# Kernel optimization log

Measured on AMD Instinct MI355X. Metric: run time of the kernel, lower is better.

## Reference

```python
import jax, jax.numpy as jnp
import numpy as np

B, C, H, W = 8, 96, 256, 256
PATCH, DIM, HEAD = 2, 384, 4
D = DIM // HEAD          # 96, minGRU feature dim
K = 2 * PATCH + 1        # 5, patch-embed kernel
GK = 3                   # positional conv kernel


def setup_inputs() -> dict:
    key = jax.random.key(0)
    ks = jax.random.split(key, 16)
    w = lambda k, shape: jax.random.normal(k, shape, jnp.float32) * 0.02
    return {
        'x': jax.random.normal(ks[0], (B, C, H, W), jnp.float32),
        'r_pw': w(ks[1], (DIM, C, K, K)),            # Conv2d weight (out,in,kh,kw)
        'r_pb': w(ks[2], (DIM,)),
        'c_pw': w(ks[3], (DIM, C, K, K)),
        'c_pb': w(ks[4], (DIM,)),
        'r_pe_w': w(ks[5], (DIM, DIM // C, GK, GK)),  # grouped conv, groups=C
        'r_pe_b': w(ks[6], (DIM,)),
        'c_pe_w': w(ks[7], (DIM, DIM // C, GK, GK)),
        'c_pe_b': w(ks[8], (DIM,)),
        'r_un_w': w(ks[9], (DIM, C, PATCH, PATCH)),   # ConvTranspose2d weight (in,out,kh,kw)
        'r_un_b': w(ks[10], (C,)),
        'c_un_w': w(ks[11], (DIM, C, PATCH, PATCH)),
        'c_un_b': w(ks[12], (C,)),
        'r_gru_w': w(ks[13], (D, 2 * D)),             # minGRU to_hidden_and_gate (no bias)
        'c_gru_w': w(ks[14], (D, 2 * D)),
    }


def _conv(x, w, b, stride, pad, groups=1):
    y = jax.lax.conv_general_dilated(
        x, w, (stride, stride), [(pad, pad), (pad, pad)],
        dimension_numbers=('NCHW', 'OIHW', 'NCHW'), feature_group_count=groups)
    return y + b[None, :, None, None]


def _min_gru(seq, w):
    # seq: (N, S, D); log-space parallel scan (heinsen scan), lucidrains minGRU
    hg = seq @ w                                  # (N, S, 2D)
    hidden, gate = jnp.split(hg, 2, axis=-1)
    log_coeffs = -jax.nn.softplus(gate)           # log(1 - z)
    log_z = -jax.nn.softplus(-gate)               # log z
    log_tilde_h = jnp.where(hidden >= 0,
                            jnp.log(jax.nn.relu(hidden) + 0.5),
                            -jax.nn.softplus(-hidden))
    a_star = jnp.cumsum(log_coeffs, axis=1)
    log_h = a_star + jax.lax.cumlogsumexp(log_z + log_tilde_h - a_star, axis=1)
    return jnp.exp(log_h)


def _unpatch(x, w, b):
    # ConvTranspose2d with kernel==stride==PATCH, pad=0: pure block expansion
    Bq, Ci, Hp, Wp = x.shape
    y = jnp.einsum('bchw,copq->bohpwq', x, w).reshape(Bq, w.shape[1], Hp * PATCH, Wp * PATCH)
    return y + b[None, :, None, None]


def reference(x, r_pw, r_pb, c_pw, c_pb, r_pe_w, r_pe_b, c_pe_w, c_pe_b,
              r_un_w, r_un_b, c_un_w, c_un_b, r_gru_w, c_gru_w):
    r = _conv(x, r_pw, r_pb, PATCH, PATCH)        # (B, DIM, Hp, Wp)
    c = _conv(x, c_pw, c_pb, PATCH, PATCH)
    r_pe = _conv(r, r_pe_w, r_pe_b, 1, 1, groups=C)
    c_pe = _conv(c, c_pe_w, c_pe_b, 1, 1, groups=C)
    Bq, _, Hp, Wp = r.shape
    # row scan: (B,head,D,Hp,Wp) -> (B,head,Wp,Hp,D) -> scan over Hp
    r = r.reshape(Bq, HEAD, D, Hp, Wp).transpose(0, 1, 4, 3, 2).reshape(-1, Hp, D)
    # col scan: (B,head,D,Hp,Wp) -> (B,head,Hp,Wp,D) -> scan over Wp
    c = c.reshape(Bq, HEAD, D, Hp, Wp).transpose(0, 1, 3, 4, 2).reshape(-1, Wp, D)
    r = _min_gru(r, r_gru_w)
    c = _min_gru(c, c_gru_w)
    r = r.reshape(Bq, HEAD, Wp, Hp, D).transpose(0, 1, 4, 3, 2).reshape(Bq, DIM, Hp, Wp)
    c = c.reshape(Bq, HEAD, Hp, Wp, D).transpose(0, 1, 4, 2, 3).reshape(Bq, DIM, Hp, Wp)
    return _unpatch(r + r_pe, r_un_w, r_un_b) + _unpatch(c + c_pe, c_un_w, c_un_b)
```

## Files before the change

kernel.cpp:

```cpp
#include <hip/hip_runtime.h>
#include <stdint.h>
#include <stdio.h>

typedef __attribute__((ext_vector_type(8))) short short8;
typedef __attribute__((ext_vector_type(4))) float f32x4;
typedef __attribute__((ext_vector_type(4))) unsigned int u32x4;
typedef __attribute__((ext_vector_type(4))) unsigned short u16x4;

#define DEV static __device__ __forceinline__

DEV unsigned short f2bf(float f){
  unsigned u = __float_as_uint(f);
  u += 0x7FFFu + ((u >> 16) & 1u);
  return (unsigned short)(u >> 16);
}
DEV float bf2f(unsigned short h){ return __uint_as_float(((unsigned)h) << 16); }

__global__ __launch_bounds__(256) void k_xt(const float* __restrict__ x,
                                            unsigned short* __restrict__ xt){
  int bid = blockIdx.x;
  int wq = bid & 3, h = (bid >> 2) & 255, b = bid >> 10;
  int w0 = wq * 64;
  __shared__ unsigned short s[64 * 104];
  int t = threadIdx.x;
  int wl = t & 63, cq = t >> 6;
  const float* xp = x + ((size_t)b * 96 * 256 + h) * 256 + w0 + wl;
  #pragma unroll
  for (int i = 0; i < 24; ++i){
    int c = cq + i * 4;
    s[wl * 104 + c] = f2bf(xp[(size_t)c * 65536]);
  }
  __syncthreads();
  unsigned short* dst = xt + (((size_t)b * 260 + h + 2) * 260 + (w0 + 2)) * 128;
  #pragma unroll
  for (int p = 0; p < 3; ++p){
    int i = t + p * 256;
    int w = i / 12, ch = i % 12;
    u32x4 v = *(const u32x4*)&s[w * 104 + ch * 8];
    *(u32x4*)&dst[(size_t)w * 128 + ch * 8] = v;
  }
}

__global__ __launch_bounds__(256) void k_pack(const float* __restrict__ rpw, const float* __restrict__ cpw,
    const float* __restrict__ runw, const float* __restrict__ cunw,
    const float* __restrict__ runb, const float* __restrict__ cunb,
    const float* __restrict__ rgw,  const float* __restrict__ cgw,
    unsigned short* __restrict__ A2, unsigned short* __restrict__ Aun,
    unsigned short* __restrict__ Agr, float* __restrict__ bun){
  int tid = blockIdx.x * 256 + threadIdx.x;
  const int NA2 = 768 * 2400, NUN = 384 * 768, NGR = 2 * 192 * 96;
  if (tid < NA2){
    int oc = tid / 2400, r = tid % 2400;
    int kh = r / 480, kw = (r / 96) % 5, ic = r % 96;
    const float* W = oc < 384 ? rpw : cpw;
    int o = oc < 384 ? oc : oc - 384;
    A2[tid] = f2bf(W[(((size_t)o * 96 + ic) * 5 + kh) * 5 + kw]);
  } else if (tid < NA2 + NUN){
    int i = tid - NA2;
    int m = i / 768, ci = i % 768;
    int co = m >> 2, p = (m >> 1) & 1, q = m & 1;
    const float* W = ci < 384 ? runw : cunw;
    int c = ci < 384 ? ci : ci - 384;
    Aun[i] = f2bf(W[(((size_t)c * 96 + co) * 2 + p) * 2 + q]);
  } else if (tid < NA2 + NUN + NGR){
    int i = tid - NA2 - NUN;
    int side = i / 18432, r = i % 18432;
    int m = r / 96, k = r % 96;
    const float* W = side ? cgw : rgw;
    Agr[i] = f2bf(W[k * 192 + m]);
  } else if (tid < NA2 + NUN + NGR + 96){
    int co = tid - NA2 - NUN - NGR;
    bun[co] = runb[co] + cunb[co];
  }
}

__global__ __launch_bounds__(512) void k_conv(const unsigned short* __restrict__ xt,
    const unsigned short* __restrict__ A2,
    const float* __restrict__ rpb, const float* __restrict__ cpb,
    unsigned short* __restrict__ cl){
  __shared__ char lds[160768];
  const int BOFF = 26624;
  const int BPITCH = 33536;
  const int BITEMS = 8384;
  int t = threadIdx.x, lane = t & 63;
  int wid = t >> 6, mw = wid >> 2, nw = wid & 3;
  int wl = lane & 15, cg = lane >> 4;
  int bid = blockIdx.x;
  int xcd = bid & 7, rr = bid >> 3;
  int mt = rr % 6, pgrp = rr / 6;
  int p = pgrp * 8 + xcd;
  int wq = p & 1, hq = (p >> 1) & 31, b = p >> 6;
  int ho0 = hq * 4, wo0 = wq * 64;
  int M0 = mt * 128;

  int a_oc = t >> 2, a_q = t & 3;
  const unsigned short* Aoc = A2 + (size_t)(M0 + a_oc) * 2400 + a_q * 24;
  char* Adst = lds + a_oc * 208 + a_q * 48;

  f32x4 acc[4][4];
  #pragma unroll
  for (int i = 0; i < 4; ++i)
    #pragma unroll
    for (int j = 0; j < 4; ++j) acc[i][j] = (f32x4){0.f, 0.f, 0.f, 0.f};

  u32x4 aR[3], bR[17];
  #pragma unroll
  for (int c = 0; c < 3; ++c) aR[c] = *(const u32x4*)(Aoc + c * 8);
  #pragma unroll
  for (int it = 0; it < 17; ++it){
    int i = t + it * 512;
    if (i < BITEMS){
      int row = i / 2096, j = i % 2096, col = j >> 4, ch = j & 15;
      bR[it] = *(const u32x4*)&xt[(((size_t)b * 260 + 2 * ho0 + 2 * row) * 260 + 2 * wo0 + col) * 128 + ch * 8];
    }
  }
  #pragma unroll
  for (int c = 0; c < 3; ++c) *(u32x4*)(Adst + c * 16) = aR[c];
  #pragma unroll
  for (int it = 0; it < 17; ++it){
    int i = t + it * 512;
    if (i < BITEMS){
      int row = i / 2096, j = i % 2096, col = j >> 4, ch = j & 15;
      *(u32x4*)(lds + BOFF + row * BPITCH + col * 256 + (ch ^ ((col >> 1) & 7)) * 16) = bR[it];
    }
  }
  __syncthreads();

  for (int kh = 0; kh < 5; ++kh){
    #pragma unroll
    for (int kw = 0; kw < 5; ++kw){
      bool last = (kh == 4 && kw == 4);
      bool khb  = (kw == 4 && kh < 4);
      if (!last){
        int nkh = kh + (kw == 4 ? 1 : 0), nkw = (kw == 4 ? 0 : kw + 1);
        const unsigned short* As = Aoc + (nkh * 5 + nkw) * 96;
        #pragma unroll
        for (int c = 0; c < 3; ++c) aR[c] = *(const u32x4*)(As + c * 8);
      }
      if (khb){
        #pragma unroll
        for (int it = 0; it < 17; ++it){
          int i = t + it * 512;
          if (i < BITEMS){
            int row = i / 2096, j = i % 2096, col = j >> 4, ch = j & 15;
            bR[it] = *(const u32x4*)&xt[(((size_t)b * 260 + 2 * ho0 + 2 * row + kh + 1) * 260 + 2 * wo0 + col) * 128 + ch * 8];
          }
        }
      }
      {
        int col = 32 * nw + 2 * wl + kw;
        int sx = (col >> 1) & 7;
        #pragma unroll
        for (int ics = 0; ics < 3; ++ics){
          short8 af[4], bfr[4];
          #pragma unroll
          for (int mf = 0; mf < 4; ++mf)
            af[mf] = *(const short8*)(lds + (mw * 64 + mf * 16 + wl) * 208 + ics * 64 + cg * 16);
          int chl = (ics * 4 + cg) ^ sx;
          #pragma unroll
          for (int nf = 0; nf < 4; ++nf)
            bfr[nf] = *(const short8*)(lds + BOFF + nf * BPITCH + col * 256 + chl * 16);
          #pragma unroll
          for (int mf = 0; mf < 4; ++mf)
            #pragma unroll
            for (int nf = 0; nf < 4; ++nf)
              acc[mf][nf] = __builtin_amdgcn_mfma_f32_16x16x32_bf16(af[mf], bfr[nf], acc[mf][nf], 0, 0, 0);
        }
      }
      __syncthreads();
      if (!last){
        #pragma unroll
        for (int c = 0; c < 3; ++c) *(u32x4*)(Adst + c * 16) = aR[c];
        if (khb){
          #pragma unroll
          for (int it = 0; it < 17; ++it){
            int i = t + it * 512;
            if (i < BITEMS){
              int row = i / 2096, j = i % 2096, col = j >> 4, ch = j & 15;
              *(u32x4*)(lds + BOFF + row * BPITCH + col * 256 + (ch ^ ((col >> 1) & 7)) * 16) = bR[it];
            }
          }
        }
      }
      __syncthreads();
    }
  }
  unsigned short* S = (unsigned short*)lds;
  #pragma unroll
  for (int mf = 0; mf < 4; ++mf)
    #pragma unroll
    for (int nf = 0; nf < 4; ++nf){
      int wol = nw * 16 + wl;
      int pxl = nf * 64 + wol;
      int sw8 = (pxl & 7) << 3;
      #pragma unroll
      for (int j = 0; j < 4; ++j){
        int ocl = mw * 64 + mf * 16 + cg * 4 + j;
        int oc = M0 + ocl;
        float v = acc[mf][nf][j] + (oc < 384 ? rpb[oc] : cpb[oc - 384]);
        S[pxl * 128 + (ocl ^ sw8)] = f2bf(v);
      }
    }
  __syncthreads();
  #pragma unroll
  for (int it = 0; it < 8; ++it){
    int i = t + it * 512;
    int pxl = i >> 4, ch = i & 15;
    int chs = ch ^ (pxl & 7);
    int ho = ho0 + (pxl >> 6), wo = wo0 + (pxl & 63);
    u32x4 v = *(const u32x4*)&S[pxl * 128 + chs * 8];
    *(u32x4*)&cl[(((size_t)b * 128 + ho) * 128 + wo) * 768 + M0 + ch * 8] = v;
  }
}

__global__ __launch_bounds__(256) void k_pe(const unsigned short* __restrict__ cl,
    const float* __restrict__ rpew, const float* __restrict__ cpew,
    const float* __restrict__ rpeb, const float* __restrict__ cpeb,
    unsigned short* __restrict__ sum){
  __shared__ unsigned short si[340 * 52];
  __shared__ float sw[48 * 36];
  __shared__ float sb[48];
  int bid = blockIdx.x;
  int wq = bid & 3, hq = (bid >> 2) & 15, slab = (bid >> 6) & 15, b = bid >> 10;
  int ch0 = slab * 48, hp0 = hq * 8, wp0 = wq * 32;
  int t = threadIdx.x;
  for (int i = t; i < 48 * 36; i += 256){
    int ocl = i / 36, r = i % 36;
    int oc = ch0 + ocl;
    const float* W = oc < 384 ? rpew : cpew;
    int o = oc < 384 ? oc : oc - 384;
    sw[i] = W[(size_t)o * 36 + r];
  }
  if (t < 48){
    int oc = ch0 + t;
    sb[t] = oc < 384 ? rpeb[oc] : cpeb[oc - 384];
  }
  for (int i = t; i < 340 * 24; i += 256){
    int pix = i / 24, c2 = i % 24;
    int r2 = pix / 34, cc = pix % 34;
    int hp = hp0 - 1 + r2, wp = wp0 - 1 + cc;
    unsigned v = 0;
    if (hp >= 0 && hp < 128 && wp >= 0 && wp < 128)
      v = *(const unsigned*)&cl[((size_t)b * 16384 + hp * 128 + wp) * 768 + ch0 + c2 * 2];
    *(unsigned*)&si[pix * 52 + c2 * 2] = v;
  }
  __syncthreads();
  int hpl = t >> 5, wpl = t & 31;
  unsigned int outp[24];
  #pragma unroll
  for (int g = 0; g < 12; ++g){
    float o0 = sb[g * 4], o1 = sb[g * 4 + 1], o2 = sb[g * 4 + 2], o3 = sb[g * 4 + 3];
    #pragma unroll
    for (int dh = 0; dh < 3; ++dh)
      #pragma unroll
      for (int dw = 0; dw < 3; ++dw){
        int pix = (hpl + dh) * 34 + (wpl + dw);
        u16x4 v = *(const u16x4*)&si[pix * 52 + g * 4];
        float x0 = bf2f(v[0]), x1 = bf2f(v[1]), x2 = bf2f(v[2]), x3 = bf2f(v[3]);
        int r = dh * 3 + dw;
        o0 = fmaf(sw[(g*4+0)*36 + 0*9 + r], x0, o0); o0 = fmaf(sw[(g*4+0)*36 + 1*9 + r], x1, o0);
        o0 = fmaf(sw[(g*4+0)*36 + 2*9 + r], x2, o0); o0 = fmaf(sw[(g*4+0)*36 + 3*9 + r], x3, o0);
        o1 = fmaf(sw[(g*4+1)*36 + 0*9 + r], x0, o1); o1 = fmaf(sw[(g*4+1)*36 + 1*9 + r], x1, o1);
        o1 = fmaf(sw[(g*4+1)*36 + 2*9 + r], x2, o1); o1 = fmaf(sw[(g*4+1)*36 + 3*9 + r], x3, o1);
        o2 = fmaf(sw[(g*4+2)*36 + 0*9 + r], x0, o2); o2 = fmaf(sw[(g*4+2)*36 + 1*9 + r], x1, o2);
        o2 = fmaf(sw[(g*4+2)*36 + 2*9 + r], x2, o2); o2 = fmaf(sw[(g*4+2)*36 + 3*9 + r], x3, o2);
        o3 = fmaf(sw[(g*4+3)*36 + 0*9 + r], x0, o3); o3 = fmaf(sw[(g*4+3)*36 + 1*9 + r], x1, o3);
        o3 = fmaf(sw[(g*4+3)*36 + 2*9 + r], x2, o3); o3 = fmaf(sw[(g*4+3)*36 + 3*9 + r], x3, o3);
      }
    outp[g * 2]     = (unsigned)f2bf(o0) | ((unsigned)f2bf(o1) << 16);
    outp[g * 2 + 1] = (unsigned)f2bf(o2) | ((unsigned)f2bf(o3) << 16);
  }
  size_t obase = (((size_t)b * 128 + hp0 + hpl) * 128 + wp0 + wpl) * 768 + ch0;
  #pragma unroll
  for (int c6 = 0; c6 < 6; ++c6){
    u32x4 v = { outp[c6 * 4], outp[c6 * 4 + 1], outp[c6 * 4 + 2], outp[c6 * 4 + 3] };
    *(u32x4*)&sum[obase + c6 * 8] = v;
  }
}

__global__ __launch_bounds__(256) void k_gruf(const unsigned short* __restrict__ cl,
    const unsigned short* __restrict__ Agr, unsigned short* __restrict__ sum){
  __shared__ char lds[78848];
  const int AOFF = 0, BOFF2 = 39936, HOFF = 53248;
  int t = threadIdx.x, lane = t & 63, wid = t >> 6;
  int wl = lane & 15, cg = lane >> 4;
  int bid = blockIdx.x;
  int cb = bid & 7, head = (bid >> 3) & 3, b = (bid >> 5) & 7, side = bid >> 8;
  size_t clbase = ((size_t)b * 16384) * 768 + side * 384 + head * 96;
  for (int i = t; i < 2304; i += 256){
    int m = i / 12, c = i % 12;
    u32x4 v = *(const u32x4*)&Agr[((size_t)side * 192 + m) * 96 + c * 8];
    *(u32x4*)(lds + AOFF + m * 208 + c * 16) = v;
  }
  for (int i = t; i < 768; i += 256){
    int px = i / 12, c = i % 12;
    int s = px >> 4, xl = px & 15;
    int xg = cb * 16 + xl;
    int pxg = side ? (xg * 128 + s) : (s * 128 + xg);
    u32x4 v = *(const u32x4*)&cl[clbase + (size_t)pxg * 768 + c * 8];
    *(u32x4*)(lds + BOFF2 + px * 208 + c * 16) = v;
  }
  int s_chain = t & 15, s_dg = t >> 4;
  float h[8];
  #pragma unroll
  for (int k = 0; k < 8; ++k) h[k] = 0.f;
  __syncthreads();

  for (int ch = 0; ch < 32; ++ch){
    int s0 = ch * 4;
    f32x4 acc[12];
    #pragma unroll
    for (int i = 0; i < 12; ++i) acc[i] = (f32x4){0.f, 0.f, 0.f, 0.f};
    #pragma unroll
    for (int ks = 0; ks < 3; ++ks){
      short8 bf = *(const short8*)(lds + BOFF2 + (wid * 16 + wl) * 208 + ks * 64 + cg * 16);
      #pragma unroll
      for (int mf = 0; mf < 12; ++mf){
        short8 af = *(const short8*)(lds + AOFF + (mf * 16 + wl) * 208 + ks * 64 + cg * 16);
        acc[mf] = __builtin_amdgcn_mfma_f32_16x16x32_bf16(af, bf, acc[mf], 0, 0, 0);
      }
    }
    {
      int px = wid * 16 + wl;
      #pragma unroll
      for (int mf = 0; mf < 12; ++mf){
        unsigned p0 = (unsigned)f2bf(acc[mf][0]) | ((unsigned)f2bf(acc[mf][1]) << 16);
        unsigned p1 = (unsigned)f2bf(acc[mf][2]) | ((unsigned)f2bf(acc[mf][3]) << 16);
        unsigned long long pp = (unsigned long long)p0 | ((unsigned long long)p1 << 32);
        *(unsigned long long*)(lds + HOFF + px * 400 + (mf * 16 + cg * 4) * 2) = pp;
      }
    }
    __syncthreads();
    if (s_dg < 12){
      #pragma unroll
      for (int s = 0; s < 4; ++s){
        int px = s * 16 + s_chain;
        short8 hid8 = *(const short8*)(lds + HOFF + px * 400 + s_dg * 16);
        short8 gat8 = *(const short8*)(lds + HOFF + px * 400 + 192 + s_dg * 16);
        int xg = cb * 16 + s_chain;
        int pxg = side ? (xg * 128 + (s0 + s)) : ((s0 + s) * 128 + xg);
        unsigned short* sp = (unsigned short*)&sum[clbase + (size_t)pxg * 768 + s_dg * 8];
        u32x4 sv = *(u32x4*)sp;
        unsigned short* svp = (unsigned short*)&sv;
        #pragma unroll
        for (int k = 0; k < 8; ++k){
          float hid = bf2f((unsigned short)hid8[k]);
          float gat = bf2f((unsigned short)gat8[k]);
          float z  = 1.f / (1.f + __expf(-gat));
          float th = hid >= 0.f ? hid + 0.5f : 1.f / (1.f + __expf(-hid));
          h[k] += z * (th - h[k]);
          svp[k] = f2bf(bf2f(svp[k]) + h[k]);
        }
        *(u32x4*)sp = sv;
      }
    }
    if (ch < 31){
      int sn = (ch + 1) * 4;
      for (int i = t; i < 768; i += 256){
        int px = i / 12, c = i % 12;
        int s = px >> 4, xl = px & 15;
        int xg = cb * 16 + xl;
        int pxg = side ? (xg * 128 + (sn + s)) : ((sn + s) * 128 + xg);
        u32x4 v = *(const u32x4*)&cl[clbase + (size_t)pxg * 768 + c * 8];
        *(u32x4*)(lds + BOFF2 + px * 208 + c * 16) = v;
      }
    }
    __syncthreads();
  }
}

__global__ __launch_bounds__(256) void k_unpatch(const unsigned short* __restrict__ sum,
    const unsigned short* __restrict__ Aun, const float* __restrict__ bun,
    float* __restrict__ out){
  __shared__ char lds[53248];
  int t = threadIdx.x, lane = t & 63;
  int wid = t >> 6, mw = wid >> 1, nw = wid & 1;
  int bid = blockIdx.x;
  int xcd = bid & 7, rr = bid >> 3;
  int mt = rr % 3, pgrp = rr / 3;
  int M0 = mt * 128;
  size_t N0 = (size_t)(pgrp * 8 + xcd) * 128;
  f32x4 acc[4][4];
  #pragma unroll
  for (int i = 0; i < 4; ++i)
    #pragma unroll
    for (int j = 0; j < 4; ++j) acc[i][j] = (f32x4){0.f, 0.f, 0.f, 0.f};
  for (int kc = 0; kc < 8; ++kc){
    __syncthreads();
    for (int i = t; i < 1536; i += 256){
      int m = i / 12, c = i % 12;
      u32x4 v = *(const u32x4*)&Aun[(size_t)(M0 + m) * 768 + kc * 96 + c * 8];
      *(u32x4*)(lds + m * 208 + c * 16) = v;
    }
    for (int i = t; i < 1536; i += 256){
      int px = i / 12, c = i % 12;
      u32x4 v = *(const u32x4*)&sum[(N0 + px) * 768 + kc * 96 + c * 8];
      *(u32x4*)(lds + 26624 + px * 208 + c * 16) = v;
    }
    __syncthreads();
    #pragma unroll
    for (int ks = 0; ks < 3; ++ks){
      short8 af[4], bfr[4];
      #pragma unroll
      for (int mf = 0; mf < 4; ++mf)
        af[mf] = *(const short8*)(lds + (mw * 64 + mf * 16 + (lane & 15)) * 208 + ks * 64 + (lane >> 4) * 16);
      #pragma unroll
      for (int nf = 0; nf < 4; ++nf)
        bfr[nf] = *(const short8*)(lds + 26624 + (nw * 64 + nf * 16 + (lane & 15)) * 208 + ks * 64 + (lane >> 4) * 16);
      #pragma unroll
      for (int mf = 0; mf < 4; ++mf)
        #pragma unroll
        for (int nf = 0; nf < 4; ++nf)
          acc[mf][nf] = __builtin_amdgcn_mfma_f32_16x16x32_bf16(af[mf], bfr[nf], acc[mf][nf], 0, 0, 0);
    }
  }
  #pragma unroll
  for (int mf = 0; mf < 4; ++mf)
    #pragma unroll
    for (int nf = 0; nf < 4; ++nf)
      #pragma unroll
      for (int j = 0; j < 4; ++j){
        int m = M0 + mw * 64 + mf * 16 + (lane >> 4) * 4 + j;
        int co = m >> 2, p = (m >> 1) & 1, q = m & 1;
        size_t px = N0 + nw * 64 + nf * 16 + (lane & 15);
        int b = (int)(px >> 14); int pxl = (int)(px & 16383);
        int hp = pxl >> 7, wp = pxl & 127;
        out[(((size_t)b * 96 + co) * 256 + 2 * hp + p) * 256 + 2 * wp + q] = acc[mf][nf][j] + bun[co];
      }
}

extern "C" void kernel_launch(void* const* d_in, const int* in_sizes, int n_in,
                              void* d_out, int out_size, void* d_ws, size_t ws_size,
                              hipStream_t stream){
  (void)in_sizes; (void)n_in; (void)out_size;
  const float* x    = (const float*)d_in[0];
  const float* rpw  = (const float*)d_in[1];
  const float* rpb  = (const float*)d_in[2];
  const float* cpw  = (const float*)d_in[3];
  const float* cpb  = (const float*)d_in[4];
  const float* rpew = (const float*)d_in[5];
  const float* rpeb = (const float*)d_in[6];
  const float* cpew = (const float*)d_in[7];
  const float* cpeb = (const float*)d_in[8];
  const float* runw = (const float*)d_in[9];
  const float* runb = (const float*)d_in[10];
  const float* cunw = (const float*)d_in[11];
  const float* cunb = (const float*)d_in[12];
  const float* rgw  = (const float*)d_in[13];
  const float* cgw  = (const float*)d_in[14];

  char* ws = (char*)d_ws;
  const size_t SZ_XT   = (size_t)8 * 260 * 260 * 128 * 2;
  const size_t OFF_A2  = SZ_XT;
  const size_t SZ_A2   = (size_t)768 * 2400 * 2;
  const size_t OFF_AUN = OFF_A2 + SZ_A2;
  const size_t SZ_AUN  = (size_t)384 * 768 * 2;
  const size_t OFF_AGR = OFF_AUN + SZ_AUN;
  const size_t SZ_AGR  = (size_t)2 * 192 * 96 * 2;
  const size_t OFF_BUN = OFF_AGR + SZ_AGR;
  const size_t OFF_HG  = ((OFF_BUN + 384) + 255) & ~(size_t)255;
  const size_t SZ_PL   = (size_t)8 * 768 * 128 * 128 * 2;
  const size_t OFF_CL  = OFF_HG + SZ_PL;
  const size_t OFF_SUM = OFF_CL + SZ_PL;
  const size_t NEED    = OFF_SUM + SZ_PL;
  if (ws_size < NEED){
    fprintf(stderr, "kernel_launch: ws_size %zu < needed %zu\n", ws_size, NEED);
    return;
  }
  unsigned short* xt  = (unsigned short*)(ws);
  unsigned short* A2  = (unsigned short*)(ws + OFF_A2);
  unsigned short* Aun = (unsigned short*)(ws + OFF_AUN);
  unsigned short* Agr = (unsigned short*)(ws + OFF_AGR);
  float*          bun = (float*)(ws + OFF_BUN);
  unsigned short* cl  = (unsigned short*)(ws + OFF_CL);
  unsigned short* sum = (unsigned short*)(ws + OFF_SUM);
  float* out = (float*)d_out;

  hipMemsetAsync(xt, 0, SZ_XT, stream);
  k_xt  <<<dim3(8192),    dim3(256), 0, stream>>>(x, xt);
  k_pack<<<dim3(8497),    dim3(256), 0, stream>>>(rpw, cpw, runw, cunw, runb, cunb, rgw, cgw, A2, Aun, Agr, bun);
  k_conv<<<dim3(3072),    dim3(512), 0, stream>>>(xt, A2, rpb, cpb, cl);
  k_pe  <<<dim3(8192),    dim3(256), 0, stream>>>(cl, rpew, cpew, rpeb, cpeb, sum);
  k_gruf<<<dim3(512),     dim3(256), 0, stream>>>(cl, Agr, sum);
  k_unpatch<<<dim3(3072), dim3(256), 0, stream>>>(sum, Aun, bun, out);
}
```

Measured before the change: 1.690 ms.

## Load conv weights directly from pre-swizzled global layout and halve conv block tile

After: 2.063 ms. 1.22x slower.

```diff
diff --git a/kernel.cpp b/kernel.cpp
--- a/kernel.cpp
+++ b/kernel.cpp
@@ -4,6 +4,7 @@
 
 typedef __attribute__((ext_vector_type(8))) short short8;
 typedef __attribute__((ext_vector_type(4))) float f32x4;
+typedef __attribute__((ext_vector_type(2))) float f32x2;
 typedef __attribute__((ext_vector_type(4))) unsigned int u32x4;
 typedef __attribute__((ext_vector_type(4))) unsigned short u16x4;
 
@@ -45,57 +46,59 @@
     const float* __restrict__ runw, const float* __restrict__ cunw,
     const float* __restrict__ runb, const float* __restrict__ cunb,
     const float* __restrict__ rgw,  const float* __restrict__ cgw,
-    unsigned short* __restrict__ A2, unsigned short* __restrict__ Aun,
+    unsigned short* __restrict__ A3, unsigned short* __restrict__ Aun,
     unsigned short* __restrict__ Agr, float* __restrict__ bun){
   int tid = blockIdx.x * 256 + threadIdx.x;
-  const int NA2 = 768 * 2400, NUN = 384 * 768, NGR = 2 * 192 * 96;
-  if (tid < NA2){
-    int oc = tid / 2400, r = tid % 2400;
-    int kh = r / 480, kw = (r / 96) % 5, ic = r % 96;
+  const int NA3 = 768 * 2400, NUN = 384 * 768, NGR = 2 * 192 * 96;
+  if (tid < NA3){
+    int e = tid & 7, lane = (tid >> 3) & 63, mf = (tid >> 9) & 3, mw = (tid >> 11) & 1;
+    int r = tid >> 12;
+    int ics = r % 3, r2 = r / 3;
+    int s = r2 % 25, mt = r2 / 25;
+    int kh = s / 5, kw = s % 5;
+    int oc = mt * 128 + mw * 64 + mf * 16 + (lane & 15);
+    int ic = ics * 32 + (lane >> 4) * 8 + e;
     const float* W = oc < 384 ? rpw : cpw;
     int o = oc < 384 ? oc : oc - 384;
-    A2[tid] = f2bf(W[(((size_t)o * 96 + ic) * 5 + kh) * 5 + kw]);
-  } else if (tid < NA2 + NUN){
-    int i = tid - NA2;
+    A3[tid] = f2bf(W[(((size_t)o * 96 + ic) * 5 + kh) * 5 + kw]);
+  } else if (tid < NA3 + NUN){
+    int i = tid - NA3;
     int m = i / 768, ci = i % 768;
     int co = m >> 2, p = (m >> 1) & 1, q = m & 1;
     const float* W = ci < 384 ? runw : cunw;
     int c = ci < 384 ? ci : ci - 384;
     Aun[i] = f2bf(W[(((size_t)c * 96 + co) * 2 + p) * 2 + q]);
-  } else if (tid < NA2 + NUN + NGR){
-    int i = tid - NA2 - NUN;
+  } else if (tid < NA3 + NUN + NGR){
+    int i = tid - NA3 - NUN;
     int side = i / 18432, r = i % 18432;
     int m = r / 96, k = r % 96;
     const float* W = side ? cgw : rgw;
     Agr[i] = f2bf(W[k * 192 + m]);
-  } else if (tid < NA2 + NUN + NGR + 96){
-    int co = tid - NA2 - NUN - NGR;
+  } else if (tid < NA3 + NUN + NGR + 96){
+    int co = tid - NA3 - NUN - NGR;
     bun[co] = runb[co] + cunb[co];
   }
 }
 
-__global__ __launch_bounds__(512) void k_conv(const unsigned short* __restrict__ xt,
-    const unsigned short* __restrict__ A2,
+__global__ __launch_bounds__(256) void k_conv(const unsigned short* __restrict__ xt,
+    const unsigned short* __restrict__ A3,
     const float* __restrict__ rpb, const float* __restrict__ cpb,
     unsigned short* __restrict__ cl){
-  __shared__ char lds[160768];
-  const int BOFF = 26624;
+  __shared__ char lds[67072];
   const int BPITCH = 33536;
-  const int BITEMS = 8384;
+  const int BITEMS = 3144;
   int t = threadIdx.x, lane = t & 63;
-  int wid = t >> 6, mw = wid >> 2, nw = wid & 3;
+  int wid = t >> 6, mw = wid >> 1, nw = wid & 1;
   int wl = lane & 15, cg = lane >> 4;
   int bid = blockIdx.x;
   int xcd = bid & 7, rr = bid >> 3;
   int mt = rr % 6, pgrp = rr / 6;
   int p = pgrp * 8 + xcd;
-  int wq = p & 1, hq = (p >> 1) & 31, b = p >> 6;
-  int ho0 = hq * 4, wo0 = wq * 64;
+  int wq = p & 1, hq = (p >> 1) & 63, b = p >> 7;
+  int ho0 = hq * 2, wo0 = wq * 64;
   int M0 = mt * 128;
 
-  int a_oc = t >> 2, a_q = t & 3;
-  const unsigned short* Aoc = A2 + (size_t)(M0 + a_oc) * 2400 + a_q * 24;
-  char* Adst = lds + a_oc * 208 + a_q * 48;
+  const unsigned short* Abase = A3 + (size_t)mt * 307200 + mw * 2048 + lane * 8;
 
   f32x4 acc[4][4];
   #pragma unroll
@@ -103,25 +106,21 @@
     #pragma unroll
     for (int j = 0; j < 4; ++j) acc[i][j] = (f32x4){0.f, 0.f, 0.f, 0.f};
 
-  u32x4 aR[3], bR[17];
-  #pragma unroll
-  for (int c = 0; c < 3; ++c) aR[c] = *(const u32x4*)(Aoc + c * 8);
-  #pragma unroll
-  for (int it = 0; it < 17; ++it){
-    int i = t + it * 512;
+  u32x4 bR[13];
+  #pragma unroll
+  for (int it = 0; it < 13; ++it){
+    int i = t + it * 256;
     if (i < BITEMS){
-      int row = i / 2096, j = i % 2096, col = j >> 4, ch = j & 15;
+      int row = i / 1572, j = i % 1572, col = j / 12, ch = j % 12;
       bR[it] = *(const u32x4*)&xt[(((size_t)b * 260 + 2 * ho0 + 2 * row) * 260 + 2 * wo0 + col) * 128 + ch * 8];
     }
   }
   #pragma unroll
-  for (int c = 0; c < 3; ++c) *(u32x4*)(Adst + c * 16) = aR[c];
-  #pragma unroll
-  for (int it = 0; it < 17; ++it){
-    int i = t + it * 512;
+  for (int it = 0; it < 13; ++it){
+    int i = t + it * 256;
     if (i < BITEMS){
-      int row = i / 2096, j = i % 2096, col = j >> 4, ch = j & 15;
-      *(u32x4*)(lds + BOFF + row * BPITCH + col * 256 + (ch ^ ((col >> 1) & 7)) * 16) = bR[it];
+      int row = i / 1572, j = i % 1572, col = j / 12, ch = j % 12;
+      *(u32x4*)(lds + row * BPITCH + col * 256 + (ch ^ ((col >> 1) & 7)) * 16) = bR[it];
     }
   }
   __syncthreads();
@@ -129,69 +128,56 @@
   for (int kh = 0; kh < 5; ++kh){
     #pragma unroll
     for (int kw = 0; kw < 5; ++kw){
-      bool last = (kh == 4 && kw == 4);
-      bool khb  = (kw == 4 && kh < 4);
-      if (!last){
-        int nkh = kh + (kw == 4 ? 1 : 0), nkw = (kw == 4 ? 0 : kw + 1);
-        const unsigned short* As = Aoc + (nkh * 5 + nkw) * 96;
-        #pragma unroll
-        for (int c = 0; c < 3; ++c) aR[c] = *(const u32x4*)(As + c * 8);
-      }
-      if (khb){
-        #pragma unroll
-        for (int it = 0; it < 17; ++it){
-          int i = t + it * 512;
+      if (kw == 4 && kh < 4){
+        #pragma unroll
+        for (int it = 0; it < 13; ++it){
+          int i = t + it * 256;
           if (i < BITEMS){
-            int row = i / 2096, j = i % 2096, col = j >> 4, ch = j & 15;
+            int row = i / 1572, j = i % 1572, col = j / 12, ch = j % 12;
             bR[it] = *(const u32x4*)&xt[(((size_t)b * 260 + 2 * ho0 + 2 * row + kh + 1) * 260 + 2 * wo0 + col) * 128 + ch * 8];
           }
         }
       }
-      {
-        int col = 32 * nw + 2 * wl + kw;
-        int sx = (col >> 1) & 7;
-        #pragma unroll
-        for (int ics = 0; ics < 3; ++ics){
-          short8 af[4], bfr[4];
-          #pragma unroll
-          for (int mf = 0; mf < 4; ++mf)
-            af[mf] = *(const short8*)(lds + (mw * 64 + mf * 16 + wl) * 208 + ics * 64 + cg * 16);
-          int chl = (ics * 4 + cg) ^ sx;
+      const unsigned short* Asl = Abase + (size_t)(kh * 5 + kw) * 12288;
+      #pragma unroll
+      for (int ics = 0; ics < 3; ++ics){
+        short8 af[4], bfr[4];
+        #pragma unroll
+        for (int mf = 0; mf < 4; ++mf)
+          af[mf] = *(const short8*)(Asl + ics * 4096 + mf * 512);
+        #pragma unroll
+        for (int nf = 0; nf < 4; ++nf){
+          int col = 32 * nf + 2 * wl + kw;
+          int chl = (ics * 4 + cg) ^ ((col >> 1) & 7);
+          bfr[nf] = *(const short8*)(lds + nw * BPITCH + col * 256 + chl * 16);
+        }
+        #pragma unroll
+        for (int mf = 0; mf < 4; ++mf)
           #pragma unroll
           for (int nf = 0; nf < 4; ++nf)
-            bfr[nf] = *(const short8*)(lds + BOFF + nf * BPITCH + col * 256 + chl * 16);
-          #pragma unroll
-          for (int mf = 0; mf < 4; ++mf)
-            #pragma unroll
-            for (int nf = 0; nf < 4; ++nf)
-              acc[mf][nf] = __builtin_amdgcn_mfma_f32_16x16x32_bf16(af[mf], bfr[nf], acc[mf][nf], 0, 0, 0);
+            acc[mf][nf] = __builtin_amdgcn_mfma_f32_16x16x32_bf16(af[mf], bfr[nf], acc[mf][nf], 0, 0, 0);
+      }
+    }
+    if (kh < 4){
+      __syncthreads();
+      #pragma unroll
+      for (int it = 0; it < 13; ++it){
+        int i = t + it * 256;
+        if (i < BITEMS){
+          int row = i / 1572, j = i % 1572, col = j / 12, ch = j % 12;
+          *(u32x4*)(lds + row * BPITCH + col * 256 + (ch ^ ((col >> 1) & 7)) * 16) = bR[it];
         }
       }
       __syncthreads();
-      if (!last){
-        #pragma unroll
-        for (int c = 0; c < 3; ++c) *(u32x4*)(Adst + c * 16) = aR[c];
-        if (khb){
-          #pragma unroll
-          for (int it = 0; it < 17; ++it){
-            int i = t + it * 512;
-            if (i < BITEMS){
-              int row = i / 2096, j = i % 2096, col = j >> 4, ch = j & 15;
-              *(u32x4*)(lds + BOFF + row * BPITCH + col * 256 + (ch ^ ((col >> 1) & 7)) * 16) = bR[it];
-            }
-          }
-        }
-      }
-      __syncthreads();
-    }
-  }
+    }
+  }
+  __syncthreads();
   unsigned short* S = (unsigned short*)lds;
   #pragma unroll
   for (int mf = 0; mf < 4; ++mf)
     #pragma unroll
     for (int nf = 0; nf < 4; ++nf){
-      int wol = nw * 16 + wl;
-      int pxl = nf * 64 + wol;
+      int pxl = nw * 64 + nf * 16 + wl;
       int sw8 = (pxl & 7) << 3;
       #pragma unroll
       for (int j = 0; j < 4; ++j){
@@ -204,7 +190,7 @@
   __syncthreads();
   #pragma unroll
   for (int it = 0; it < 8; ++it){
-    int i = t + it * 512;
+    int i = t + it * 256;
     int pxl = i >> 4, ch = i & 15;
     int chs = ch ^ (pxl & 7);
     int ho = ho0 + (pxl >> 6), wo = wo0 + (pxl & 63);
@@ -417,16 +403,19 @@
   #pragma unroll
   for (int mf = 0; mf < 4; ++mf)
     #pragma unroll
-    for (int nf = 0; nf < 4; ++nf)
-      #pragma unroll
-      for (int j = 0; j < 4; ++j){
-        int m = M0 + mw * 64 + mf * 16 + (lane >> 4) * 4 + j;
-        int co = m >> 2, p = (m >> 1) & 1, q = m & 1;
-        size_t px = N0 + nw * 64 + nf * 16 + (lane & 15);
-        int b = (int)(px >> 14); int pxl = (int)(px & 16383);
-        int hp = pxl >> 7, wp = pxl & 127;
-        out[(((size_t)b * 96 + co) * 256 + 2 * hp + p) * 256 + 2 * wp + q] = acc[mf][nf][j] + bun[co];
-      }
+    for (int nf = 0; nf < 4; ++nf){
+      int m = M0 + mw * 64 + mf * 16 + (lane >> 4) * 4;
+      int co = m >> 2;
+      size_t px = N0 + nw * 64 + nf * 16 + (lane & 15);
+      int b = (int)(px >> 14); int pxl = (int)(px & 16383);
+      int hp = pxl >> 7, wp = pxl & 127;
+      float bias = bun[co];
+      f32x2 v01 = { acc[mf][nf][0] + bias, acc[mf][nf][1] + bias };
+      f32x2 v23 = { acc[mf][nf][2] + bias, acc[mf][nf][3] + bias };
+      size_t ob = (((size_t)b * 96 + co) * 256 + 2 * hp) * 256 + 2 * wp;
+      *(f32x2*)&out[ob]       = v01;
+      *(f32x2*)&out[ob + 256] = v23;
+    }
 }
 
 extern "C" void kernel_launch(void* const* d_in, const int* in_sizes, int n_in,
@@ -451,9 +440,9 @@
 
   char* ws = (char*)d_ws;
   const size_t SZ_XT   = (size_t)8 * 260 * 260 * 128 * 2;
-  const size_t OFF_A2  = SZ_XT;
-  const size_t SZ_A2   = (size_t)768 * 2400 * 2;
-  const size_t OFF_AUN = OFF_A2 + SZ_A2;
+  const size_t OFF_A3  = SZ_XT;
+  const size_t SZ_A3   = (size_t)768 * 2400 * 2;
+  const size_t OFF_AUN = OFF_A3 + SZ_A3;
   const size_t SZ_AUN  = (size_t)384 * 768 * 2;
   const size_t OFF_AGR = OFF_AUN + SZ_AUN;
   const size_t SZ_AGR  = (size_t)2 * 192 * 96 * 2;
@@ -468,7 +457,7 @@
     return;
   }
   unsigned short* xt  = (unsigned short*)(ws);
-  unsigned short* A2  = (unsigned short*)(ws + OFF_A2);
+  unsigned short* A3  = (unsigned short*)(ws + OFF_A3);
   unsigned short* Aun = (unsigned short*)(ws + OFF_AUN);
   unsigned short* Agr = (unsigned short*)(ws + OFF_AGR);
   float*          bun = (float*)(ws + OFF_BUN);
@@ -478,8 +467,8 @@
 
   hipMemsetAsync(xt, 0, SZ_XT, stream);
   k_xt  <<<dim3(8192),    dim3(256), 0, stream>>>(x, xt);
-  k_pack<<<dim3(8497),    dim3(256), 0, stream>>>(rpw, cpw, runw, cunw, runb, cunb, rgw, cgw, A2, Aun, Agr, bun);
-  k_conv<<<dim3(3072),    dim3(512), 0, stream>>>(xt, A2, rpb, cpb, cl);
+  k_pack<<<dim3(8497),    dim3(256), 0, stream>>>(rpw, cpw, runw, cunw, runb, cunb, rgw, cgw, A3, Aun, Agr, bun);
+  k_conv<<<dim3(6144),    dim3(256), 0, stream>>>(xt, A3, rpb, cpb, cl);
   k_pe  <<<dim3(8192),    dim3(256), 0, stream>>>(cl, rpew, cpew, rpeb, cpeb, sum);
   k_gruf<<<dim3(512),     dim3(256), 0, stream>>>(cl, Agr, sum);
   k_unpatch<<<dim3(3072), dim3(256), 0, stream>>>(sum, Aun, bun, out);
```
